# Performance work log

Measured on AMD Instinct MI355X. Metric: run time of the kernel, lower is better.

Reference implementation:

```python
import jax, jax.numpy as jnp
import numpy as np

BINS = 30
MOMENTUM = 0.75
LOSS_WEIGHT = 1.0


def setup_inputs() -> dict:
    key = jax.random.key(0)
    k1, k2 = jax.random.split(key)
    N, C = 8192, 2048
    preds = jax.random.normal(k1, (N, C), dtype=jnp.float32)
    targets = jax.random.randint(k2, (N, C), 0, 2).astype(jnp.int32)  # binary multi-hot
    acc_sum = jnp.zeros((BINS, C), dtype=jnp.float32)  # EMA histogram state
    return {"preds": preds, "targets": targets, "acc_sum": acc_sum}


def reference(preds, targets, acc_sum):
    N, C = preds.shape
    t = targets.astype(preds.dtype)

    # gradient norm g = |sigmoid(p) - t|, detached (weights carry no grad)
    g = jnp.abs(jax.nn.sigmoid(jax.lax.stop_gradient(preds)) - t)

    # bin index: edges[i] = i/BINS, so bin = floor(g*BINS), g=1.0 -> last bin (edge[-1]+=1e-6)
    bin_idx = jnp.clip(jnp.floor(g * BINS).astype(jnp.int32), 0, BINS - 1)  # [N, C]

    # per-label histogram: counts[b, c] = #examples with bin b in column c
    cols = jnp.broadcast_to(jnp.arange(C, dtype=jnp.int32)[None, :], (N, C))
    counts = jnp.zeros((BINS, C), dtype=preds.dtype).at[bin_idx, cols].add(1.0)

    # n[c] = number of non-empty bins for label c
    n = jnp.sum(counts >= 1.0, axis=0).astype(preds.dtype)  # [C]

    # EMA update of the histogram (momentum > 0 branch)
    acc_new = MOMENTUM * acc_sum + (1.0 - MOMENTUM) * counts  # [BINS, C]

    tot = jnp.asarray(float(max(N, 1.0)), preds.dtype)
    weights = tot / acc_new[bin_idx, cols]               # gather per-element density
    weights = weights / jnp.maximum(n, 1.0)[None, :]      # normalize by #valid bins
    weights = jax.lax.stop_gradient(weights)

    # BCE with logits, elementwise: softplus-style stable form
    bce = jnp.logaddexp(0.0, preds) - preds * t
    loss = jnp.mean(weights * bce)
    return loss * LOSS_WEIGHT
```

## Files before the change

kernel.cpp:

```cpp
#include <hip/hip_runtime.h>

#define BINS  30
#define NROWS 8192
#define NCOLS 2048
#define YSLICES 32
#define COLS_PER_BLK 128
#define ROWS_PER_BLK (NROWS / YSLICES)

#define FIXED_SCALE 1048576.0f
#define SUM_MASK    ((1ull << 54) - 1)

#define WS_PART_CNT 0
#define WS_PART_SUM (YSLICES * BINS * NCOLS * 4)
#define WS_COUNTS   (2 * YSLICES * BINS * NCOLS * 4)
#define WS_BCESUM   (WS_COUNTS + BINS * NCOLS * 4)
#define WS_BPART    (WS_BCESUM + BINS * NCOLS * 4)

__global__ __launch_bounds__(1024, 8) void k_main(
    const float* __restrict__ preds, const int* __restrict__ targets,
    float* __restrict__ part_cnt, float* __restrict__ part_sum)
{
    __shared__ unsigned long long h_pack[BINS * COLS_PER_BLK];
    const int tid = threadIdx.x;
    for (int i = tid; i < BINS * COLS_PER_BLK; i += 1024) h_pack[i] = 0ull;
    __syncthreads();

    const int colBase = blockIdx.x * COLS_PER_BLK;
    const int wave = tid >> 6;
    const int lane = tid & 63;
    const int hl   = lane & 31;
    const int rp   = lane >> 5;
    const int r0   = blockIdx.y * ROWS_PER_BLK + wave * 2 + rp;
    const int col0 = colBase + 4 * hl;

    const int NIT = ROWS_PER_BLK / 32;
    size_t base = (size_t)r0 * NCOLS + col0;

    float4 p_cur = *(const float4*)(preds + base);
    int4   t_cur = *(const int4*)(targets + base);

    #pragma unroll
    for (int k = 0; k < NIT; ++k) {
        base += (k < NIT - 1) ? (size_t)(32 * NCOLS) : 0;
        float4 p_nxt = *(const float4*)(preds + base);
        int4   t_nxt = *(const int4*)(targets + base);

        const float pv[4] = {p_cur.x, p_cur.y, p_cur.z, p_cur.w};
        const int   tv[4] = {t_cur.x, t_cur.y, t_cur.z, t_cur.w};
        #pragma unroll
        for (int j = 0; j < 4; ++j) {
            float p  = pv[j];
            float pp = tv[j] ? -p : p;
            float e  = __expf(-fabsf(pp));
            float d  = 1.0f + e;
            float r1 = __builtin_amdgcn_rcpf(d);
            float g  = (pp >= 0.0f) ? r1 : e * r1;
            int   b  = (int)(g * 30.0f);
            b = b > (BINS - 1) ? (BINS - 1) : b;
            float bce = fmaxf(pp, 0.0f) + __logf(d);
            unsigned long long pk =
                (1ull << 54) | (unsigned long long)(unsigned)(bce * FIXED_SCALE + 0.5f);
            const int s = b * COLS_PER_BLK + j * 32 + hl;
            atomicAdd(&h_pack[s], pk);
        }
        p_cur = p_nxt;
        t_cur = t_nxt;
    }
    __syncthreads();

    const size_t outBase = (size_t)blockIdx.y * BINS * NCOLS;
    for (int i = tid; i < BINS * COLS_PER_BLK; i += 1024) {
        const unsigned long long v = h_pack[i];
        const int b = i >> 7;
        const int s = i & 127;
        const int col = colBase + ((s & 31) << 2) + (s >> 5);
        const size_t o = outBase + (size_t)b * NCOLS + col;
        part_cnt[o] = (float)(unsigned)(v >> 54);
        part_sum[o] = (float)(v & SUM_MASK) * (1.0f / FIXED_SCALE);
    }
}

__global__ __launch_bounds__(256) void k_reduce(
    const float* __restrict__ part_cnt, const float* __restrict__ part_sum,
    float* __restrict__ counts, float* __restrict__ bceSum)
{
    const int id = blockIdx.x * 256 + threadIdx.x;
    float c = 0.0f, s = 0.0f;
    #pragma unroll 8
    for (int y = 0; y < YSLICES; ++y) {
        c += part_cnt[(size_t)y * BINS * NCOLS + id];
        s += part_sum[(size_t)y * BINS * NCOLS + id];
    }
    counts[id] = c;
    bceSum[id] = s;
}

__global__ __launch_bounds__(256) void k_colsum(
    const float* __restrict__ counts, const float* __restrict__ bceSum,
    const float* __restrict__ acc_sum, float* __restrict__ blockPart)
{
    __shared__ float wave_sums[4];
    const int tid = threadIdx.x;
    const int c   = blockIdx.x * 256 + tid;

    float colsum = 0.0f;
    int n = 0;
    #pragma unroll
    for (int b = 0; b < BINS; ++b) {
        const size_t gidx = (size_t)b * NCOLS + c;
        float cnt = counts[gidx];
        if (cnt >= 1.0f) {
            n += 1;
            float acc_new = 0.75f * acc_sum[gidx] + 0.25f * cnt;
            colsum += bceSum[gidx] / acc_new;
        }
    }
    colsum /= (float)((n > 1 ? n : 1) * NCOLS);

    #pragma unroll
    for (int off = 32; off > 0; off >>= 1)
        colsum += __shfl_down(colsum, off, 64);
    if ((tid & 63) == 0) wave_sums[tid >> 6] = colsum;
    __syncthreads();
    if (tid == 0)
        blockPart[blockIdx.x] = wave_sums[0] + wave_sums[1] + wave_sums[2] + wave_sums[3];
}

__global__ void k_final(const float* __restrict__ blockPart, float* __restrict__ out)
{
    double s = 0.0;
    #pragma unroll
    for (int i = 0; i < 8; ++i) s += (double)blockPart[i];
    out[0] = (float)s;
}

extern "C" void kernel_launch(void* const* d_in, const int* in_sizes, int n_in,
                              void* d_out, int out_size, void* d_ws, size_t ws_size,
                              hipStream_t stream)
{
    const float* preds   = (const float*)d_in[0];
    const int*   targets = (const int*)d_in[1];
    const float* acc_sum = (const float*)d_in[2];

    float* part_cnt  = (float*)((char*)d_ws + WS_PART_CNT);
    float* part_sum  = (float*)((char*)d_ws + WS_PART_SUM);
    float* counts    = (float*)((char*)d_ws + WS_COUNTS);
    float* bceSum    = (float*)((char*)d_ws + WS_BCESUM);
    float* blockPart = (float*)((char*)d_ws + WS_BPART);

    dim3 gA(NCOLS / COLS_PER_BLK, YSLICES);
    k_main<<<gA, 1024, 0, stream>>>(preds, targets, part_cnt, part_sum);

    k_reduce<<<(BINS * NCOLS) / 256, 256, 0, stream>>>(part_cnt, part_sum, counts, bceSum);

    k_colsum<<<NCOLS / 256, 256, 0, stream>>>(counts, bceSum, acc_sum, blockPart);

    k_final<<<1, 1, 0, stream>>>(blockPart, (float*)d_out);
}
```

Before: 181.4 us.

## Merge per-slice histograms via global 64-bit atomics and drop reduce kernel

Blocks now cover 256 columns by 128 rows (a 8x64 grid) and flush their shared packed histogram straight into a single global 64-bit array with atomicAdd, skipping empty bins. This removes the 32-slice partial buffers and the separate reduce kernel, cutting workspace traffic and one launch. The fixed-point encoding changes to a 50-bit sum field with a 2^24 scale, and a memset is added to zero the global array. The costs are global atomic contention from 64 row-blocks per column and a tighter overflow margin on the packed sum.

```diff
diff --git a/kernel.cpp b/kernel.cpp
--- a/kernel.cpp
+++ b/kernel.cpp
@@ -3,100 +3,80 @@
 #define BINS  30
 #define NROWS 8192
 #define NCOLS 2048
-#define YSLICES 32
-#define COLS_PER_BLK 128
-#define ROWS_PER_BLK (NROWS / YSLICES)
+#define COLS_PER_BLK 256
+#define ROWS_PER_BLK 128
 
-#define FIXED_SCALE 1048576.0f
-#define SUM_MASK    ((1ull << 54) - 1)
+#define FIXED_SCALE 16777216.0f
+#define CNT_SHIFT   50
+#define SUM_MASK    ((1ull << CNT_SHIFT) - 1)
 
-#define WS_PART_CNT 0
-#define WS_PART_SUM (YSLICES * BINS * NCOLS * 4)
-#define WS_COUNTS   (2 * YSLICES * BINS * NCOLS * 4)
-#define WS_BCESUM   (WS_COUNTS + BINS * NCOLS * 4)
-#define WS_BPART    (WS_BCESUM + BINS * NCOLS * 4)
+#define WS_GPACK 0
+#define WS_BPART (BINS * NCOLS * 8)
 
 __global__ __launch_bounds__(1024, 8) void k_main(
     const float* __restrict__ preds, const int* __restrict__ targets,
-    float* __restrict__ part_cnt, float* __restrict__ part_sum)
+    unsigned long long* __restrict__ g_pack)
 {
-    __shared__ unsigned long long h_pack[BINS * COLS_PER_BLK];
+    __shared__ unsigned long long h[BINS * COLS_PER_BLK];
     const int tid = threadIdx.x;
-    for (int i = tid; i < BINS * COLS_PER_BLK; i += 1024) h_pack[i] = 0ull;
+    for (int i = tid; i < BINS * COLS_PER_BLK; i += 1024) h[i] = 0ull;
     __syncthreads();
 
-    const int colBase = blockIdx.x * COLS_PER_BLK;
     const int wave = tid >> 6;
     const int lane = tid & 63;
-    const int hl   = lane & 31;
-    const int rp   = lane >> 5;
-    const int r0   = blockIdx.y * ROWS_PER_BLK + wave * 2 + rp;
-    const int col0 = colBase + 4 * hl;
+    const int colBase = blockIdx.x * COLS_PER_BLK;
+    const int col0 = colBase + 4 * lane;
+    const int r0   = blockIdx.y * ROWS_PER_BLK + wave * 8;
 
-    const int NIT = ROWS_PER_BLK / 32;
-    size_t base = (size_t)r0 * NCOLS + col0;
-
-    float4 p_cur = *(const float4*)(preds + base);
-    int4   t_cur = *(const int4*)(targets + base);
+    const float4* P = (const float4*)(preds   + (size_t)r0 * NCOLS + col0);
+    const int4*   T = (const int4*)  (targets + (size_t)r0 * NCOLS + col0);
+    const int RV = NCOLS / 4;
 
     #pragma unroll
-    for (int k = 0; k < NIT; ++k) {
-        base += (k < NIT - 1) ? (size_t)(32 * NCOLS) : 0;
-        float4 p_nxt = *(const float4*)(preds + base);
-        int4   t_nxt = *(const int4*)(targets + base);
+    for (int batch = 0; batch < 2; ++batch) {
+        float4 p0 = P[0], p1 = P[RV], p2 = P[2 * RV], p3 = P[3 * RV];
+        int4   t0 = T[0], t1 = T[RV], t2 = T[2 * RV], t3 = T[3 * RV];
+        P += 4 * RV; T += 4 * RV;
 
-        const float pv[4] = {p_cur.x, p_cur.y, p_cur.z, p_cur.w};
-        const int   tv[4] = {t_cur.x, t_cur.y, t_cur.z, t_cur.w};
+        const float4 pb[4] = {p0, p1, p2, p3};
+        const int4   tb[4] = {t0, t1, t2, t3};
         #pragma unroll
-        for (int j = 0; j < 4; ++j) {
-            float p  = pv[j];
-            float pp = tv[j] ? -p : p;
-            float e  = __expf(-fabsf(pp));
-            float d  = 1.0f + e;
-            float r1 = __builtin_amdgcn_rcpf(d);
-            float g  = (pp >= 0.0f) ? r1 : e * r1;
-            int   b  = (int)(g * 30.0f);
-            b = b > (BINS - 1) ? (BINS - 1) : b;
-            float bce = fmaxf(pp, 0.0f) + __logf(d);
-            unsigned long long pk =
-                (1ull << 54) | (unsigned long long)(unsigned)(bce * FIXED_SCALE + 0.5f);
-            const int s = b * COLS_PER_BLK + j * 32 + hl;
-            atomicAdd(&h_pack[s], pk);
+        for (int q = 0; q < 4; ++q) {
+            const float pv[4] = {pb[q].x, pb[q].y, pb[q].z, pb[q].w};
+            const int   tv[4] = {tb[q].x, tb[q].y, tb[q].z, tb[q].w};
+            #pragma unroll
+            for (int j = 0; j < 4; ++j) {
+                float p  = pv[j];
+                float pp = tv[j] ? -p : p;
+                float e  = __expf(-fabsf(pp));
+                float d  = 1.0f + e;
+                float r1 = __builtin_amdgcn_rcpf(d);
+                float g  = (pp >= 0.0f) ? r1 : e * r1;
+                int   b  = (int)(g * 30.0f);
+                b = b > (BINS - 1) ? (BINS - 1) : b;
+                float bce = fmaxf(pp, 0.0f) + __logf(d);
+                unsigned long long pk = (1ull << CNT_SHIFT)
+                    | (unsigned long long)(bce * FIXED_SCALE + 0.5f);
+                atomicAdd(&h[b * COLS_PER_BLK + (j << 6) + lane], pk);
+            }
         }
-        p_cur = p_nxt;
-        t_cur = t_nxt;
     }
     __syncthreads();
 
-    const size_t outBase = (size_t)blockIdx.y * BINS * NCOLS;
     for (int i = tid; i < BINS * COLS_PER_BLK; i += 1024) {
-        const unsigned long long v = h_pack[i];
-        const int b = i >> 7;
-        const int s = i & 127;
-        const int col = colBase + ((s & 31) << 2) + (s >> 5);
-        const size_t o = outBase + (size_t)b * NCOLS + col;
-        part_cnt[o] = (float)(unsigned)(v >> 54);
-        part_sum[o] = (float)(v & SUM_MASK) * (1.0f / FIXED_SCALE);
+        const unsigned long long v = h[i];
+        if (v) {
+            const int b = i >> 8;
+            const int r = i & 255;
+            const int j = r >> 6;
+            const int l = r & 63;
+            atomicAdd(&g_pack[(size_t)b * NCOLS + colBase + 4 * l + j], v);
+        }
     }
 }
 
-__global__ __launch_bounds__(256) void k_reduce(
-    const float* __restrict__ part_cnt, const float* __restrict__ part_sum,
-    float* __restrict__ counts, float* __restrict__ bceSum)
-{
-    const int id = blockIdx.x * 256 + threadIdx.x;
-    float c = 0.0f, s = 0.0f;
-    #pragma unroll 8
-    for (int y = 0; y < YSLICES; ++y) {
-        c += part_cnt[(size_t)y * BINS * NCOLS + id];
-        s += part_sum[(size_t)y * BINS * NCOLS + id];
-    }
-    counts[id] = c;
-    bceSum[id] = s;
-}
-
 __global__ __launch_bounds__(256) void k_colsum(
-    const float* __restrict__ counts, const float* __restrict__ bceSum,
+    const unsigned long long* __restrict__ g_pack,
     const float* __restrict__ acc_sum, float* __restrict__ blockPart)
 {
     __shared__ float wave_sums[4];
@@ -108,11 +88,13 @@
     #pragma unroll
     for (int b = 0; b < BINS; ++b) {
         const size_t gidx = (size_t)b * NCOLS + c;
-        float cnt = counts[gidx];
-        if (cnt >= 1.0f) {
+        const unsigned long long v = g_pack[gidx];
+        if (v) {
             n += 1;
+            float cnt = (float)(unsigned)(v >> CNT_SHIFT);
+            float s   = (float)(v & SUM_MASK) * (1.0f / FIXED_SCALE);
             float acc_new = 0.75f * acc_sum[gidx] + 0.25f * cnt;
-            colsum += bceSum[gidx] / acc_new;
+            colsum += s / acc_new;
         }
     }
     colsum /= (float)((n > 1 ? n : 1) * NCOLS);
@@ -142,18 +124,15 @@
     const int*   targets = (const int*)d_in[1];
     const float* acc_sum = (const float*)d_in[2];
 
-    float* part_cnt  = (float*)((char*)d_ws + WS_PART_CNT);
-    float* part_sum  = (float*)((char*)d_ws + WS_PART_SUM);
-    float* counts    = (float*)((char*)d_ws + WS_COUNTS);
-    float* bceSum    = (float*)((char*)d_ws + WS_BCESUM);
-    float* blockPart = (float*)((char*)d_ws + WS_BPART);
+    unsigned long long* g_pack = (unsigned long long*)((char*)d_ws + WS_GPACK);
+    float* blockPart           = (float*)((char*)d_ws + WS_BPART);
 
-    dim3 gA(NCOLS / COLS_PER_BLK, YSLICES);
-    k_main<<<gA, 1024, 0, stream>>>(preds, targets, part_cnt, part_sum);
+    hipMemsetAsync(g_pack, 0, BINS * NCOLS * 8, stream);
 
-    k_reduce<<<(BINS * NCOLS) / 256, 256, 0, stream>>>(part_cnt, part_sum, counts, bceSum);
+    dim3 gA(NCOLS / COLS_PER_BLK, NROWS / ROWS_PER_BLK);
+    k_main<<<gA, 1024, 0, stream>>>(preds, targets, g_pack);
 
-    k_colsum<<<NCOLS / 256, 256, 0, stream>>>(counts, bceSum, acc_sum, blockPart);
+    k_colsum<<<NCOLS / 256, 256, 0, stream>>>(g_pack, acc_sum, blockPart);
 
     k_final<<<1, 1, 0, stream>>>(blockPart, (float*)d_out);
 }
```

New measurement: 251.4 us. +38.5%, slower.
